# Optimization experiments

Hardware: AMD Instinct MI355X
Metric: run time of the kernel (lower is better)

Reference implementation:

```python
import jax, jax.numpy as jnp
import numpy as np

B_TRIALS = 64   # n_trials
DZ = 512        # latent / network dim
DU = 16         # input dim
DX = 256        # observation dim
T = 1000        # time steps
DECAY = 0.9
G = np.sqrt(2.0)


def setup_inputs() -> dict:
    key = jax.random.key(0)
    k0, k1, k2, k3, k4 = jax.random.split(key, 5)
    z0 = jax.random.normal(k0, (B_TRIALS, DZ), jnp.float32)
    v = jax.random.normal(k1, (B_TRIALS, DU, T), jnp.float32)
    # W ~ (1-decay) * g / sqrt(dz) * N(0,1), per Transition_FullRank init
    W = ((1.0 - DECAY) * G / np.sqrt(DZ)) * jax.random.normal(k2, (DZ, DZ), jnp.float32)
    # Wu: uniform init scaled by 1/sqrt(du)
    Wu = (jax.random.uniform(k3, (DZ, DU), jnp.float32) * 2.0 - 1.0) / np.sqrt(DU)
    h = jnp.zeros((DZ,), jnp.float32)
    # decay_param = log(-log(decay))
    decay_param = jnp.full((1,), np.log(-np.log(DECAY)), jnp.float32)
    # Affine_observation: B ~ sqrt(2/(dz+dv)) * N(0,1), dv=0
    B_obs = np.sqrt(2.0 / DZ) * jax.random.normal(k4, (DZ, DX), jnp.float32)
    Bias = jnp.zeros((DX,), jnp.float32)
    return dict(z0=z0, v=v, W=W, Wu=Wu, h=h, decay_param=decay_param,
                B_obs=B_obs, Bias=Bias)


def reference(z0, v, W, Wu, h, decay_param, B_obs, Bias):
    # decay = exp(-exp(decay_param))
    decay = jnp.exp(-jnp.exp(decay_param[0]))
    v_seq = jnp.transpose(v, (2, 0, 1))  # [T, B, du]

    def step(z, vt):
        # z' = decay*z + W @ relu(z - h) + Wu @ v_t  (per trial)
        z_new = decay * z + jax.nn.relu(z - h) @ W.T + vt @ Wu.T
        return z_new, z_new

    _, zs = jax.lax.scan(step, z0, v_seq)      # [T, B, dz]
    zs = jnp.transpose(zs, (1, 2, 0))          # [B, dz, T]
    # Affine_observation (identity nonlinearity): einsum('zx,bzt->bxt') + bias
    x = jnp.einsum('zx,bzt->bxt', B_obs, zs) + Bias[None, :, None]
    return x
```

## Files before the change

### kernel.cpp

```cpp
#include <hip/hip_runtime.h>

#define DZc 512
#define Bc  64
#define Tc  1000
#define DUc 16
#define DXc 256
#define AROW 552


typedef __attribute__((ext_vector_type(4))) float f32x4;
typedef __attribute__((ext_vector_type(8))) short s16x8;
typedef __attribute__((ext_vector_type(4))) unsigned u32x4;

__device__ __forceinline__ unsigned short f2bf(float x) {
  unsigned u = __builtin_bit_cast(unsigned, x);
  u = u + 0x7FFFu + ((u >> 16) & 1u);
  return (unsigned short)(u >> 16);
}
__device__ __forceinline__ float bf2f(unsigned short u) {
  unsigned x = ((unsigned)u) << 16;
  return __builtin_bit_cast(float, x);
}
__device__ __forceinline__ unsigned cvt_pk_bf16(float lo, float hi) {
  unsigned r;
  asm("v_cvt_pk_bf16_f32 %0, %1, %2" : "=v"(r) : "v"(lo), "v"(hi));
  return r;
}
__device__ __forceinline__ float dpp_swap1(float x) {
  int r = __builtin_amdgcn_mov_dpp(__builtin_bit_cast(int, x), 0xB1, 0xF, 0xF, true);
  return __builtin_bit_cast(float, r);
}

__global__ void pack_w_kernel(const float* __restrict__ W,
                              const float* __restrict__ Wu,
                              unsigned short* __restrict__ Wp) {
  int d = blockIdx.x * 256 + threadIdx.x;
  int j = d & 7, l = (d >> 3) & 63, nt = (d >> 9) & 31, kt = d >> 14;
  int n = nt * 16 + (l & 15);
  int k = kt * 32 + ((l >> 4) << 3) + j;
  float val = (k < DZc) ? W[n * DZc + k] : Wu[n * DUc + (k & 15)];
  Wp[d] = f2bf(val);
}

__global__ void pack_b_kernel(const float* __restrict__ B,
                              unsigned short* __restrict__ Bp) {
  int d = blockIdx.x * 256 + threadIdx.x;
  int j = d & 7, l = (d >> 3) & 63, nt = (d >> 9) & 15, kt = d >> 13;
  int n = nt * 16 + (l & 15);
  int k = kt * 32 + ((l >> 4) << 3) + j;
  Bp[d] = f2bf(B[k * DXc + n]);
}

__global__ __launch_bounds__(512, 2) void rnn_rec_kernel(
    const float* __restrict__ z0, const float* __restrict__ v,
    const float* __restrict__ h, const float* __restrict__ dp,
    const unsigned short* __restrict__ Wp, unsigned short* __restrict__ zs,
    unsigned int* __restrict__ cnts) {
  __shared__ __align__(16) unsigned short abuf[2][16][AROW];

  const int bid = blockIdx.x;
  const int g = bid & 7;
  const int s = bid >> 3;
  if (g >= 4) return;
  const int tid = threadIdx.x;
  const int lane = tid & 63;
  const int w = tid >> 6;
  const int l15 = lane & 15;
  const int lg = lane >> 4;
  const int b0 = g * 16;
  const int nbase = s * 256 + w * 32;

  s16x8 wr[34];
#pragma unroll
  for (int kt = 0; kt < 17; ++kt) {
#pragma unroll
    for (int ntl = 0; ntl < 2; ++ntl) {
      int nt = s * 16 + w * 2 + ntl;
      wr[kt * 2 + ntl] =
          *(const s16x8*)(Wp + ((size_t)((kt * 32 + nt) * 64 + lane)) * 8);
    }
  }

  float hreg[2];
  f32x4 acc[2];
#pragma unroll
  for (int ntl = 0; ntl < 2; ++ntl) {
    hreg[ntl] = h[nbase + ntl * 16 + l15];
#pragma unroll
    for (int r = 0; r < 4; ++r)
      acc[ntl][r] = z0[(size_t)(b0 + lg * 4 + r) * DZc + nbase + ntl * 16 + l15];
  }
  const float decay = expf(-expf(dp[0]));

  const int ptrial = tid >> 5;
  const int koff = (tid & 31) * 8;
  const int pk = (1 - s) * 256 + koff;
  float hpart[8];
#pragma unroll
  for (int j = 0; j < 8; ++j) hpart[j] = h[pk + j];

  const int du = tid & 15, trr = tid >> 4;
  const size_t vbase = ((size_t)(b0 + trr) * DUc + du) * Tc;
  float vcur = (tid < 256) ? v[vbase] : 0.f;

#pragma unroll
  for (int half = 0; half < 2; ++half) {
    int kk = half * 256 + koff;
    const float* zp = z0 + (size_t)(b0 + ptrial) * DZc + kk;
    s16x8 ov;
#pragma unroll
    for (int j = 0; j < 8; ++j) {
      float av = zp[j] - h[kk + j];
      ov[j] = (short)f2bf(av > 0.f ? av : 0.f);
    }
    *(s16x8*)&abuf[0][ptrial][kk] = ov;
  }
  if (tid < 256) {
    unsigned short hi = f2bf(vcur);
    abuf[0][trr][512 + du] = hi;
    abuf[0][trr][528 + du] = f2bf(vcur - bf2f(hi));
  }

  unsigned int* mycnt = cnts + (g * 2 + s) * 16;
  const unsigned int* pcnt = cnts + (g * 2 + (s ^ 1)) * 16;
  unsigned* zs32 = (unsigned*)zs;

  int p = 0;
  for (int t = 0; t < Tc; ++t) {
    float vnext = (tid < 256) ? v[vbase + (t + 1 < Tc ? t + 1 : Tc - 1)] : 0.f;
#pragma unroll
    for (int ntl = 0; ntl < 2; ++ntl)
#pragma unroll
      for (int r = 0; r < 4; ++r) acc[ntl][r] *= decay;

    if (t > 0) {
      int iters = 0;
      while (__hip_atomic_load(pcnt, __ATOMIC_RELAXED,
                               __HIP_MEMORY_SCOPE_AGENT) < (unsigned)(8 * t)) {
        __builtin_amdgcn_s_sleep(2);
        if (++iters > (1 << 22)) break;
      }
      asm volatile("" ::: "memory");
      u32x4 pz4 = *(const u32x4*)(zs32 +
            ((size_t)(t - 1) * Bc + b0 + ptrial) * 256 + (pk >> 1));
      u32x4 av;
#pragma unroll
      for (int j2 = 0; j2 < 4; ++j2) {
        unsigned wd = pz4[j2];
        float lo = __builtin_bit_cast(float, wd << 16);
        float hi = __builtin_bit_cast(float, wd & 0xFFFF0000u);
        lo = lo - hpart[j2 * 2];
        hi = hi - hpart[j2 * 2 + 1];
        lo = lo > 0.f ? lo : 0.f;
        hi = hi > 0.f ? hi : 0.f;
        av[j2] = cvt_pk_bf16(lo, hi);
      }
      *(u32x4*)&abuf[p][ptrial][pk] = av;
    }

    asm volatile("s_waitcnt lgkmcnt(0)\n\ts_barrier" ::: "memory");

#pragma unroll
    for (int kt = 0; kt < 17; ++kt) {
      s16x8 af = *(const s16x8*)&abuf[p][l15][kt * 32 + lg * 8];
      acc[0] = __builtin_amdgcn_mfma_f32_16x16x32_bf16(af, wr[kt * 2 + 0], acc[0], 0, 0, 0);
      acc[1] = __builtin_amdgcn_mfma_f32_16x16x32_bf16(af, wr[kt * 2 + 1], acc[1], 0, 0, 0);
    }

    const size_t zrow0 = (size_t)t * Bc + b0 + lg * 4;
#pragma unroll
    for (int r = 0; r < 4; ++r) {
      float d0 = dpp_swap1(acc[0][r]);
      float d1 = dpp_swap1(acc[1][r]);
      if (!(lane & 1)) {
        unsigned c0 = cvt_pk_bf16(acc[0][r], d0);
        unsigned c1 = cvt_pk_bf16(acc[1][r], d1);
        unsigned* dst = zs32 + (zrow0 + r) * 256 + (nbase >> 1) + (l15 >> 1);
        __hip_atomic_store(dst, c0, __ATOMIC_RELAXED, __HIP_MEMORY_SCOPE_AGENT);
        __hip_atomic_store(dst + 8, c1, __ATOMIC_RELAXED, __HIP_MEMORY_SCOPE_AGENT);
      }
    }

#pragma unroll
    for (int r = 0; r < 4; ++r) {
      float a0 = acc[0][r] - hreg[0]; a0 = a0 > 0.f ? a0 : 0.f;
      float a1 = acc[1][r] - hreg[1]; a1 = a1 > 0.f ? a1 : 0.f;
      float d0 = dpp_swap1(a0);
      float d1 = dpp_swap1(a1);
      if (!(lane & 1)) {
        unsigned c0 = cvt_pk_bf16(a0, d0);
        unsigned c1 = cvt_pk_bf16(a1, d1);
        *(unsigned*)&abuf[p ^ 1][lg * 4 + r][nbase + (l15 & ~1)] = c0;
        *(unsigned*)&abuf[p ^ 1][lg * 4 + r][nbase + 16 + (l15 & ~1)] = c1;
      }
    }
    if (tid < 256) {
      unsigned short hi = f2bf(vnext);
      abuf[p ^ 1][trr][512 + du] = hi;
      abuf[p ^ 1][trr][528 + du] = f2bf(vnext - bf2f(hi));
    }

    asm volatile("s_waitcnt vmcnt(0)" ::: "memory");
    if (lane == 0)
      __hip_atomic_fetch_add((unsigned*)mycnt, 1u, __ATOMIC_RELAXED,
                             __HIP_MEMORY_SCOPE_AGENT);
    p ^= 1;
    vcur = vnext;
  }
}

__global__ __launch_bounds__(256, 1) void rnn_proj_kernel(
    const unsigned short* __restrict__ zs, const unsigned short* __restrict__ Bp,
    const float* __restrict__ Bias, float* __restrict__ x) {
  const int wg = blockIdx.x;
  const int b = wg / 63;
  const int tbase = (wg % 63) * 16;
  const int tid = threadIdx.x;
  const int lane = tid & 63;
  const int w = tid >> 6;
  const int l15 = lane & 15, lg = lane >> 4;

  const int trow = tbase + l15;
  const int trc = trow < Tc ? trow : Tc - 1;
  const unsigned short* abase = zs + ((size_t)trc * Bc + b) * DZc + lg * 8;
  const s16x8 zz = {0, 0, 0, 0, 0, 0, 0, 0};

  f32x4 acc[4];
#pragma unroll
  for (int n = 0; n < 4; ++n)
#pragma unroll
    for (int e = 0; e < 4; ++e) acc[n][e] = 0.f;

#pragma unroll
  for (int kt = 0; kt < 16; ++kt) {
    s16x8 af = *(const s16x8*)(abase + kt * 32);
    af = (trow < Tc) ? af : zz;
#pragma unroll
    for (int n = 0; n < 4; ++n) {
      s16x8 bf = *(const s16x8*)(Bp + (size_t)((kt * 16 + w * 4 + n) * 64 + lane) * 8);
      acc[n] = __builtin_amdgcn_mfma_f32_16x16x32_bf16(af, bf, acc[n], 0, 0, 0);
    }
  }

  const int t = tbase + lg * 4;
  if (t < Tc) {
#pragma unroll
    for (int n = 0; n < 4; ++n) {
      int xo = (w * 4 + n) * 16 + l15;
      float bias = Bias[xo];
      f32x4 val = acc[n];
#pragma unroll
      for (int e = 0; e < 4; ++e) val[e] += bias;
      *(f32x4*)(x + ((size_t)b * DXc + xo) * Tc + t) = val;
    }
  }
}

extern "C" void kernel_launch(void* const* d_in, const int* in_sizes, int n_in,
                              void* d_out, int out_size, void* d_ws, size_t ws_size,
                              hipStream_t stream) {
  const float* z0   = (const float*)d_in[0];
  const float* v    = (const float*)d_in[1];
  const float* W    = (const float*)d_in[2];
  const float* Wu   = (const float*)d_in[3];
  const float* h    = (const float*)d_in[4];
  const float* dp   = (const float*)d_in[5];
  const float* Bo   = (const float*)d_in[6];
  const float* Bias = (const float*)d_in[7];
  float* x = (float*)d_out;

  unsigned short* Wp = (unsigned short*)d_ws;
  unsigned short* Bp = Wp + 278528;
  unsigned short* zs = Bp + 131072;
  unsigned int* cnts = (unsigned int*)(zs + 32768000);

  hipMemsetAsync(cnts, 0, 128 * sizeof(unsigned int), stream);
  pack_w_kernel<<<1088, 256, 0, stream>>>(W, Wu, Wp);
  pack_b_kernel<<<512, 256, 0, stream>>>(Bo, Bp);
  rnn_rec_kernel<<<16, 512, 0, stream>>>(z0, v, h, dp, Wp, zs, cnts);
  rnn_proj_kernel<<<4032, 256, 0, stream>>>(zs, Bp, Bias, x);
}
```

Baseline: 2.333 ms.

## Exchange fp32 partial sums between paired blocks instead of bf16 states

Each block of a pair now owns half of the K dimension (its own half of z) rather than receiving the partner's z half. It computes partial products for the partner's output columns, publishes them as fp32 through a global exchange buffer, and signals before it computes its own columns, which overlaps the handshake with its own MFMA work. The grid shrinks from 16 launched blocks (half exiting immediately) to 8, and the input-weight tile moves into LDS. This adds a global fp32 round-trip each step and a different rounding path, since partials are summed in fp32 rather than built from re-quantized bf16 z.

New measurement: 4.243 ms. +81.9%, slower.

```diff
diff --git a/kernel.cpp b/kernel.cpp
--- a/kernel.cpp
+++ b/kernel.cpp
@@ -5,12 +5,12 @@
 #define Tc  1000
 #define DUc 16
 #define DXc 256
-#define AROW 552
+#define AROW 296
 
 
 typedef __attribute__((ext_vector_type(4))) float f32x4;
 typedef __attribute__((ext_vector_type(8))) short s16x8;
-typedef __attribute__((ext_vector_type(4))) unsigned u32x4;
+typedef unsigned long long u64;
 
 __device__ __forceinline__ unsigned short f2bf(float x) {
   unsigned u = __builtin_bit_cast(unsigned, x);
@@ -55,13 +55,13 @@
     const float* __restrict__ z0, const float* __restrict__ v,
     const float* __restrict__ h, const float* __restrict__ dp,
     const unsigned short* __restrict__ Wp, unsigned short* __restrict__ zs,
-    unsigned int* __restrict__ cnts) {
+    unsigned int* __restrict__ cnts, u64* __restrict__ pxc) {
   __shared__ __align__(16) unsigned short abuf[2][16][AROW];
+  __shared__ __align__(16) unsigned short wlds[8][2][512];
 
   const int bid = blockIdx.x;
-  const int g = bid & 7;
-  const int s = bid >> 3;
-  if (g >= 4) return;
+  const int g = bid >> 1;
+  const int s = bid & 1;
   const int tid = threadIdx.x;
   const int lane = tid & 63;
   const int w = tid >> 6;
@@ -69,16 +69,27 @@
   const int lg = lane >> 4;
   const int b0 = g * 16;
   const int nbase = s * 256 + w * 32;
-
-  s16x8 wr[34];
-#pragma unroll
-  for (int kt = 0; kt < 17; ++kt) {
+  const int s8 = s * 8;
+
+  s16x8 wr[32];
+#pragma unroll
+  for (int ktl = 0; ktl < 8; ++ktl) {
 #pragma unroll
     for (int ntl = 0; ntl < 2; ++ntl) {
-      int nt = s * 16 + w * 2 + ntl;
-      wr[kt * 2 + ntl] =
-          *(const s16x8*)(Wp + ((size_t)((kt * 32 + nt) * 64 + lane)) * 8);
-    }
+      int ktg = s8 + ktl;
+      int ntA = (1 - s) * 16 + w * 2 + ntl;
+      int ntB = s * 16 + w * 2 + ntl;
+      wr[ktl * 2 + ntl] =
+          *(const s16x8*)(Wp + ((size_t)((ktg * 32 + ntA) * 64 + lane)) * 8);
+      wr[16 + ktl * 2 + ntl] =
+          *(const s16x8*)(Wp + ((size_t)((ktg * 32 + ntB) * 64 + lane)) * 8);
+    }
+  }
+#pragma unroll
+  for (int ntl = 0; ntl < 2; ++ntl) {
+    int ntB = s * 16 + w * 2 + ntl;
+    s16x8 f = *(const s16x8*)(Wp + ((size_t)((16 * 32 + ntB) * 64 + lane)) * 8);
+    *(s16x8*)&wlds[w][ntl][lane * 8] = f;
   }
 
   float hreg[2];
@@ -92,39 +103,34 @@
   }
   const float decay = expf(-expf(dp[0]));
 
-  const int ptrial = tid >> 5;
-  const int koff = (tid & 31) * 8;
-  const int pk = (1 - s) * 256 + koff;
-  float hpart[8];
-#pragma unroll
-  for (int j = 0; j < 8; ++j) hpart[j] = h[pk + j];
-
-  const int du = tid & 15, trr = tid >> 4;
-  const size_t vbase = ((size_t)(b0 + trr) * DUc + du) * Tc;
+  const int du = tid & 15, trV = tid >> 4;
+  const size_t vbase = ((size_t)(b0 + trV) * DUc + du) * Tc;
   float vcur = (tid < 256) ? v[vbase] : 0.f;
 
-#pragma unroll
-  for (int half = 0; half < 2; ++half) {
-    int kk = half * 256 + koff;
-    const float* zp = z0 + (size_t)(b0 + ptrial) * DZc + kk;
+  {
+    const int trI = tid >> 5;
+    const int koff = (tid & 31) * 8;
+    const float* zp = z0 + (size_t)(b0 + trI) * DZc + s * 256 + koff;
     s16x8 ov;
 #pragma unroll
     for (int j = 0; j < 8; ++j) {
-      float av = zp[j] - h[kk + j];
+      float av = zp[j] - h[s * 256 + koff + j];
       ov[j] = (short)f2bf(av > 0.f ? av : 0.f);
     }
-    *(s16x8*)&abuf[0][ptrial][kk] = ov;
+    *(s16x8*)&abuf[0][trI][koff] = ov;
   }
   if (tid < 256) {
     unsigned short hi = f2bf(vcur);
-    abuf[0][trr][512 + du] = hi;
-    abuf[0][trr][528 + du] = f2bf(vcur - bf2f(hi));
+    abuf[0][trV][256 + du] = hi;
+    abuf[0][trV][272 + du] = f2bf(vcur - bf2f(hi));
   }
 
   unsigned int* mycnt = cnts + (g * 2 + s) * 16;
   const unsigned int* pcnt = cnts + (g * 2 + (s ^ 1)) * 16;
   unsigned* zs32 = (unsigned*)zs;
 
+  const int pxoff = (lg * 4) * 128 + (w * 2) * 8 + (l15 >> 1);
+
   int p = 0;
   for (int t = 0; t < Tc; ++t) {
     float vnext = (tid < 256) ? v[vbase + (t + 1 < Tc ? t + 1 : Tc - 1)] : 0.f;
@@ -133,38 +139,80 @@
 #pragma unroll
       for (int r = 0; r < 4; ++r) acc[ntl][r] *= decay;
 
-    if (t > 0) {
+    asm volatile("s_waitcnt lgkmcnt(0)\n\ts_barrier" ::: "memory");
+
+    s16x8 af[8];
+    f32x4 accP[2];
+#pragma unroll
+    for (int ntl = 0; ntl < 2; ++ntl)
+#pragma unroll
+      for (int r = 0; r < 4; ++r) accP[ntl][r] = 0.f;
+#pragma unroll
+    for (int ktl = 0; ktl < 8; ++ktl) {
+      af[ktl] = *(const s16x8*)&abuf[p][l15][ktl * 32 + lg * 8];
+      accP[0] = __builtin_amdgcn_mfma_f32_16x16x32_bf16(af[ktl], wr[ktl * 2 + 0], accP[0], 0, 0, 0);
+      accP[1] = __builtin_amdgcn_mfma_f32_16x16x32_bf16(af[ktl], wr[ktl * 2 + 1], accP[1], 0, 0, 0);
+    }
+    {
+      u64* dstp = pxc + (size_t)(((t & 1) * 4 + g) * 2 + s) * 2048 + pxoff;
+#pragma unroll
+      for (int ntl = 0; ntl < 2; ++ntl)
+#pragma unroll
+        for (int r = 0; r < 4; ++r) {
+          float lo = accP[ntl][r];
+          float hi = dpp_swap1(lo);
+          if (!(lane & 1)) {
+            u64 q = (u64)__builtin_bit_cast(unsigned, lo) |
+                    ((u64)__builtin_bit_cast(unsigned, hi) << 32);
+            __hip_atomic_store(dstp + r * 128 + ntl * 8, q,
+                               __ATOMIC_RELAXED, __HIP_MEMORY_SCOPE_AGENT);
+          }
+        }
+    }
+    asm volatile("s_waitcnt vmcnt(0)" ::: "memory");
+    if (lane == 0)
+      __hip_atomic_fetch_add((unsigned*)mycnt, 1u, __ATOMIC_RELAXED,
+                             __HIP_MEMORY_SCOPE_AGENT);
+
+#pragma unroll
+    for (int ktl = 0; ktl < 8; ++ktl) {
+      acc[0] = __builtin_amdgcn_mfma_f32_16x16x32_bf16(af[ktl], wr[16 + ktl * 2 + 0], acc[0], 0, 0, 0);
+      acc[1] = __builtin_amdgcn_mfma_f32_16x16x32_bf16(af[ktl], wr[16 + ktl * 2 + 1], acc[1], 0, 0, 0);
+    }
+    {
+      s16x8 afv = *(const s16x8*)&abuf[p][l15][256 + lg * 8];
+      s16x8 bv0 = *(const s16x8*)&wlds[w][0][lane * 8];
+      s16x8 bv1 = *(const s16x8*)&wlds[w][1][lane * 8];
+      acc[0] = __builtin_amdgcn_mfma_f32_16x16x32_bf16(afv, bv0, acc[0], 0, 0, 0);
+      acc[1] = __builtin_amdgcn_mfma_f32_16x16x32_bf16(afv, bv1, acc[1], 0, 0, 0);
+    }
+
+    {
       int iters = 0;
       while (__hip_atomic_load(pcnt, __ATOMIC_RELAXED,
-                               __HIP_MEMORY_SCOPE_AGENT) < (unsigned)(8 * t)) {
+                               __HIP_MEMORY_SCOPE_AGENT) < (unsigned)(8 * (t + 1))) {
         __builtin_amdgcn_s_sleep(2);
         if (++iters > (1 << 22)) break;
       }
       asm volatile("" ::: "memory");
-      u32x4 pz4 = *(const u32x4*)(zs32 +
-            ((size_t)(t - 1) * Bc + b0 + ptrial) * 256 + (pk >> 1));
-      u32x4 av;
-#pragma unroll
-      for (int j2 = 0; j2 < 4; ++j2) {
-        unsigned wd = pz4[j2];
-        float lo = __builtin_bit_cast(float, wd << 16);
-        float hi = __builtin_bit_cast(float, wd & 0xFFFF0000u);
-        lo = lo - hpart[j2 * 2];
-        hi = hi - hpart[j2 * 2 + 1];
-        lo = lo > 0.f ? lo : 0.f;
-        hi = hi > 0.f ? hi : 0.f;
-        av[j2] = cvt_pk_bf16(lo, hi);
-      }
-      *(u32x4*)&abuf[p][ptrial][pk] = av;
-    }
-
-    asm volatile("s_waitcnt lgkmcnt(0)\n\ts_barrier" ::: "memory");
-
-#pragma unroll
-    for (int kt = 0; kt < 17; ++kt) {
-      s16x8 af = *(const s16x8*)&abuf[p][l15][kt * 32 + lg * 8];
-      acc[0] = __builtin_amdgcn_mfma_f32_16x16x32_bf16(af, wr[kt * 2 + 0], acc[0], 0, 0, 0);
-      acc[1] = __builtin_amdgcn_mfma_f32_16x16x32_bf16(af, wr[kt * 2 + 1], acc[1], 0, 0, 0);
+      const u64* srcp = pxc + (size_t)(((t & 1) * 4 + g) * 2 + (s ^ 1)) * 2048 + pxoff;
+      u64 q[2][4];
+#pragma unroll
+      for (int ntl = 0; ntl < 2; ++ntl)
+#pragma unroll
+        for (int r = 0; r < 4; ++r)
+          if (!(lane & 1))
+            q[ntl][r] = __hip_atomic_load(srcp + r * 128 + ntl * 8,
+                                          __ATOMIC_RELAXED, __HIP_MEMORY_SCOPE_AGENT);
+#pragma unroll
+      for (int ntl = 0; ntl < 2; ++ntl)
+#pragma unroll
+        for (int r = 0; r < 4; ++r) {
+          float lo = __builtin_bit_cast(float, (unsigned)q[ntl][r]);
+          float hiw = __builtin_bit_cast(float, (unsigned)(q[ntl][r] >> 32));
+          float sw = dpp_swap1(hiw);
+          acc[ntl][r] += (lane & 1) ? sw : lo;
+        }
     }
 
     const size_t zrow0 = (size_t)t * Bc + b0 + lg * 4;
@@ -173,11 +221,9 @@
       float d0 = dpp_swap1(acc[0][r]);
       float d1 = dpp_swap1(acc[1][r]);
       if (!(lane & 1)) {
-        unsigned c0 = cvt_pk_bf16(acc[0][r], d0);
-        unsigned c1 = cvt_pk_bf16(acc[1][r], d1);
         unsigned* dst = zs32 + (zrow0 + r) * 256 + (nbase >> 1) + (l15 >> 1);
-        __hip_atomic_store(dst, c0, __ATOMIC_RELAXED, __HIP_MEMORY_SCOPE_AGENT);
-        __hip_atomic_store(dst + 8, c1, __ATOMIC_RELAXED, __HIP_MEMORY_SCOPE_AGENT);
+        dst[0] = cvt_pk_bf16(acc[0][r], d0);
+        dst[8] = cvt_pk_bf16(acc[1][r], d1);
       }
     }
 
@@ -188,22 +234,18 @@
       float d0 = dpp_swap1(a0);
       float d1 = dpp_swap1(a1);
       if (!(lane & 1)) {
-        unsigned c0 = cvt_pk_bf16(a0, d0);
-        unsigned c1 = cvt_pk_bf16(a1, d1);
-        *(unsigned*)&abuf[p ^ 1][lg * 4 + r][nbase + (l15 & ~1)] = c0;
-        *(unsigned*)&abuf[p ^ 1][lg * 4 + r][nbase + 16 + (l15 & ~1)] = c1;
+        *(unsigned*)&abuf[p ^ 1][lg * 4 + r][w * 32 + (l15 & ~1)] =
+            cvt_pk_bf16(a0, d0);
+        *(unsigned*)&abuf[p ^ 1][lg * 4 + r][w * 32 + 16 + (l15 & ~1)] =
+            cvt_pk_bf16(a1, d1);
       }
     }
     if (tid < 256) {
       unsigned short hi = f2bf(vnext);
-      abuf[p ^ 1][trr][512 + du] = hi;
-      abuf[p ^ 1][trr][528 + du] = f2bf(vnext - bf2f(hi));
-    }
-
-    asm volatile("s_waitcnt vmcnt(0)" ::: "memory");
-    if (lane == 0)
-      __hip_atomic_fetch_add((unsigned*)mycnt, 1u, __ATOMIC_RELAXED,
-                             __HIP_MEMORY_SCOPE_AGENT);
+      abuf[p ^ 1][trV][256 + du] = hi;
+      abuf[p ^ 1][trV][272 + du] = f2bf(vnext - bf2f(hi));
+    }
+
     p ^= 1;
     vcur = vnext;
   }
@@ -273,10 +315,11 @@
   unsigned short* Bp = Wp + 278528;
   unsigned short* zs = Bp + 131072;
   unsigned int* cnts = (unsigned int*)(zs + 32768000);
+  u64* pxc = (u64*)(cnts + 128);
 
   hipMemsetAsync(cnts, 0, 128 * sizeof(unsigned int), stream);
   pack_w_kernel<<<1088, 256, 0, stream>>>(W, Wu, Wp);
   pack_b_kernel<<<512, 256, 0, stream>>>(Bo, Bp);
-  rnn_rec_kernel<<<16, 512, 0, stream>>>(z0, v, h, dp, Wp, zs, cnts);
+  rnn_rec_kernel<<<8, 512, 0, stream>>>(z0, v, h, dp, Wp, zs, cnts, pxc);
   rnn_proj_kernel<<<4032, 256, 0, stream>>>(zs, Bp, Bias, x);
 }
```
